# Kernel optimization log

Measured on AMD Instinct MI355X. Metric: run time of the kernel, lower is better.

## Reference

```python
import jax, jax.numpy as jnp
import numpy as np


def _gaussian_splat_map(mask, sigma_x, sigma_y):
    """Equivalent to the torch scatter loop: for every pixel (p,q) with mask>0,
    add exp(-((i-p)^2/(2 sx^2) + (j-q)^2/(2 sy^2))) into map[b]. Because the
    Gaussian is separable, the sum over sources is exactly Gx @ M @ Gy with
    full HxH / WxW Gaussian distance kernels. Then normalize by per-batch max
    (max==0 -> 1)."""
    B, H, W = mask.shape
    ih = jnp.arange(H, dtype=jnp.float32)
    iw = jnp.arange(W, dtype=jnp.float32)
    dx = ih[:, None] - ih[None, :]                      # (H, H): i - p
    dy = iw[:, None] - iw[None, :]                      # (W, W): q - j (symmetric)
    Gx = jnp.exp(-(dx * dx) / (2.0 * sigma_x * sigma_x))
    Gy = jnp.exp(-(dy * dy) / (2.0 * sigma_y * sigma_y))
    m = (mask > 0).astype(jnp.float32)                  # (B, H, W) source indicator
    g = jnp.einsum('ip,bpq,qj->bij', Gx, m, Gy)         # summed Gaussians per batch
    mx = jnp.max(g, axis=(1, 2), keepdims=True)
    mx = jnp.where(mx == 0, jnp.float32(1.0), mx)
    return g / mx


def setup_inputs() -> dict:
    key = jax.random.key(0)
    B, C, H, W = 64, 4, 256, 256
    x = jax.random.normal(key, (B, C, H, W), dtype=jnp.float32)
    return {"x": x}


def reference(x):
    # x: (B, 4, H, W) -> output: (B, 5, H, W) with history=True, mul=True
    ch0 = x[:, 0, :, :]
    target = _gaussian_splat_map(x[:, 2, :, :], 1.0, 1.0)
    cost = _gaussian_splat_map(x[:, 1, :, :], 1.0, 1.0)
    hist = _gaussian_splat_map(x[:, 3, :, :], 0.5, 0.5)
    mul = target * cost
    return jnp.stack([ch0, target, cost, hist, mul], axis=1)
```

## Files before the change

### kernel.cpp

```cpp
#include <hip/hip_runtime.h>
#include <cmath>

#define HH 256
#define WW 256
#define BB 64
#define RR 4
#define OROWS 16
#define TROWS (OROWS + 2*RR)
#define TSTR 260

static __device__ __forceinline__ float bin(float v) { return (v > 0.0f) ? 1.0f : 0.0f; }

__global__ __launch_bounds__(256) void splat_kernel(const float* __restrict__ x,
                                                    float* __restrict__ out,
                                                    float* __restrict__ maxws) {
    __shared__ float tmp[TROWS * TSTR];
    __shared__ float wred[4];

    const int strip = blockIdx.x;
    const int z = blockIdx.y;
    const int b = z / 3;
    const int m = z - 3 * b;
    const int src_c = (m == 0) ? 2 : ((m == 1) ? 1 : 3);
    const float inv2s2 = (m == 2) ? 2.0f : 0.5f;

    float w[RR + 1];
#pragma unroll
    for (int d = 0; d <= RR; ++d) w[d] = expf(-(float)(d * d) * inv2s2);

    const int ti0 = strip * OROWS;
    const float* xc = x + (((size_t)b * 4 + src_c) << 16);
    const int tid = threadIdx.x;

#pragma unroll
    for (int t = 0; t < 3; ++t) {
        int idx = tid + t * 256;
        int r = idx >> 5;
        int g = idx & 31;
        int gi = ti0 + r - RR;
        float4 q0 = make_float4(0.f,0.f,0.f,0.f), q1 = q0, q2 = q0, q3 = q0;
        if (gi >= 0 && gi < HH) {
            const float4* row = (const float4*)(xc + ((size_t)gi << 8));
            int i0 = (g > 0) ? (2 * g - 1) : 0;
            int i3 = (g < 31) ? (2 * g + 2) : 63;
            q0 = row[i0];
            q1 = row[2 * g];
            q2 = row[2 * g + 1];
            q3 = row[i3];
            if (g == 0)  q0 = make_float4(0.f,0.f,0.f,0.f);
            if (g == 31) q3 = make_float4(0.f,0.f,0.f,0.f);
        }
        float a[16] = {bin(q0.x), bin(q0.y), bin(q0.z), bin(q0.w),
                       bin(q1.x), bin(q1.y), bin(q1.z), bin(q1.w),
                       bin(q2.x), bin(q2.y), bin(q2.z), bin(q2.w),
                       bin(q3.x), bin(q3.y), bin(q3.z), bin(q3.w)};
        float o[8];
#pragma unroll
        for (int j = 0; j < 8; ++j) {
            o[j] = w[4] * (a[j]     + a[j + 8])
                 + w[3] * (a[j + 1] + a[j + 7])
                 + w[2] * (a[j + 2] + a[j + 6])
                 + w[1] * (a[j + 3] + a[j + 5])
                 + w[0] *  a[j + 4];
        }
        float* trow = &tmp[r * TSTR + 8 * g];
        *(float4*)trow       = make_float4(o[0], o[1], o[2], o[3]);
        *(float4*)(trow + 4) = make_float4(o[4], o[5], o[6], o[7]);
    }
    __syncthreads();

    const int c = tid & 63;
    const int gr = tid >> 6;
    float4 acc[4];
#pragma unroll
    for (int rr = 0; rr < 4; ++rr) acc[rr] = make_float4(0.f,0.f,0.f,0.f);
#pragma unroll
    for (int k = 0; k < 12; ++k) {
        float4 v = *(const float4*)&tmp[(4 * gr + k) * TSTR + 4 * c];
#pragma unroll
        for (int rr = 0; rr < 4; ++rr) {
            int d = k - RR - rr;
            if (d >= -RR && d <= RR) {
                float wk = w[d < 0 ? -d : d];
                acc[rr].x += wk * v.x; acc[rr].y += wk * v.y;
                acc[rr].z += wk * v.z; acc[rr].w += wk * v.w;
            }
        }
    }

    float* oc = out + (((size_t)b * 5 + (m + 1)) << 16);
    float lmax = 0.0f;
#pragma unroll
    for (int rr = 0; rr < 4; ++rr) {
        int row = ti0 + 4 * gr + rr;
        *(float4*)&oc[((size_t)row << 8) + 4 * c] = acc[rr];
        lmax = fmaxf(lmax, fmaxf(fmaxf(acc[rr].x, acc[rr].y), fmaxf(acc[rr].z, acc[rr].w)));
    }

#pragma unroll
    for (int off = 32; off > 0; off >>= 1)
        lmax = fmaxf(lmax, __shfl_down(lmax, off, 64));
    if ((tid & 63) == 0) wred[tid >> 6] = lmax;
    __syncthreads();
    if (tid == 0)
        maxws[z * 16 + strip] = fmaxf(fmaxf(wred[0], wred[1]), fmaxf(wred[2], wred[3]));
}

__global__ __launch_bounds__(256) void finalize_kernel(const float* __restrict__ x,
                                                       float* __restrict__ out,
                                                       const float* __restrict__ maxws) {
    __shared__ float lds[48];
    const int b = blockIdx.x >> 3;
    const int slab = blockIdx.x & 7;
    const int tid = threadIdx.x;

    if (tid < 48) lds[tid] = maxws[b * 48 + tid];
    __syncthreads();

    float mt = 0.f, mc = 0.f, mh = 0.f;
#pragma unroll
    for (int s = 0; s < 16; ++s) {
        mt = fmaxf(mt, lds[s]);
        mc = fmaxf(mc, lds[16 + s]);
        mh = fmaxf(mh, lds[32 + s]);
    }
    if (mt == 0.f) mt = 1.f;
    if (mc == 0.f) mc = 1.f;
    if (mh == 0.f) mh = 1.f;
    const float rt = 1.f / mt, rc = 1.f / mc, rh = 1.f / mh;

    const int plane4 = HH * WW / 4;
    const float4* x0 = (const float4*)(x + ((size_t)b * 4 << 16));
    float4* o = (float4*)(out + ((size_t)b * 5 << 16));

#pragma unroll
    for (int i = 0; i < 8; ++i) {
        int q = slab * 2048 + i * 256 + tid;
        float4 c0 = x0[q];
        float4 t = o[plane4 + q];
        float4 c = o[2 * plane4 + q];
        float4 h = o[3 * plane4 + q];
        t.x *= rt; t.y *= rt; t.z *= rt; t.w *= rt;
        c.x *= rc; c.y *= rc; c.z *= rc; c.w *= rc;
        h.x *= rh; h.y *= rh; h.z *= rh; h.w *= rh;
        float4 mul = make_float4(t.x * c.x, t.y * c.y, t.z * c.z, t.w * c.w);
        o[q] = c0;
        o[plane4 + q] = t;
        o[2 * plane4 + q] = c;
        o[3 * plane4 + q] = h;
        o[4 * plane4 + q] = mul;
    }
}

extern "C" void kernel_launch(void* const* d_in, const int* in_sizes, int n_in,
                              void* d_out, int out_size, void* d_ws, size_t ws_size,
                              hipStream_t stream) {
    const float* x = (const float*)d_in[0];
    float* out = (float*)d_out;
    float* maxws = (float*)d_ws;

    dim3 g1(HH / OROWS, BB * 3);
    hipLaunchKernelGGL(splat_kernel, g1, dim3(256), 0, stream, x, out, maxws);

    hipLaunchKernelGGL(finalize_kernel, dim3(BB * 8), dim3(256), 0, stream, x, out, maxws);
}
```

Baseline: 154.9 us.

## Stage unnormalized splat maps in bf16 workspace and enlarge row strips

The splat kernel now writes the unnormalized maps as bf16 into a separate workspace instead of fp32 into the output, which halves the intermediate write and read-back traffic between the two kernels. The finalize kernel reads the bf16 maps, normalizes them and writes all fp32 output planes once. Strips grow from 16 to 32 rows, which lowers the halo overhead per block but halves the number of blocks. Rounding to bf16 adds error of up to about 0.4% relative, which may fail tight tolerances.

New measurement: 156.7 us. Within noise of the previous version (+1.2%).

```diff
diff --git a/kernel.cpp b/kernel.cpp
--- a/kernel.cpp
+++ b/kernel.cpp
@@ -1,18 +1,30 @@
 #include <hip/hip_runtime.h>
+#include <hip/hip_bf16.h>
 #include <cmath>
 
 #define HH 256
 #define WW 256
 #define BB 64
 #define RR 4
-#define OROWS 16
+#define OROWS 32
+#define NSTRIP (HH / OROWS)
 #define TROWS (OROWS + 2*RR)
 #define TSTR 260
+#define MAPS_BYTES ((size_t)3 * BB * HH * WW * 2)
 
 static __device__ __forceinline__ float bin(float v) { return (v > 0.0f) ? 1.0f : 0.0f; }
 
+static __device__ __forceinline__ unsigned pk_bf16(float a, float b) {
+    __hip_bfloat162 h = __float22bfloat162_rn(make_float2(a, b));
+    return *reinterpret_cast<unsigned*>(&h);
+}
+static __device__ __forceinline__ float2 up_bf16(unsigned u) {
+    __hip_bfloat162 h = *reinterpret_cast<__hip_bfloat162*>(&u);
+    return __bfloat1622float2(h);
+}
+
 __global__ __launch_bounds__(256) void splat_kernel(const float* __restrict__ x,
-                                                    float* __restrict__ out,
+                                                    unsigned short* __restrict__ maps,
                                                     float* __restrict__ maxws) {
     __shared__ float tmp[TROWS * TSTR];
     __shared__ float wred[4];
@@ -33,7 +45,7 @@
     const int tid = threadIdx.x;
 
 #pragma unroll
-    for (int t = 0; t < 3; ++t) {
+    for (int t = 0; t < 5; ++t) {
         int idx = tid + t * 256;
         int r = idx >> 5;
         int g = idx & 31;
@@ -70,15 +82,15 @@
     __syncthreads();
 
     const int c = tid & 63;
-    const int gr = tid >> 6;
-    float4 acc[4];
+    const int wv = tid >> 6;
+    float4 acc[8];
 #pragma unroll
-    for (int rr = 0; rr < 4; ++rr) acc[rr] = make_float4(0.f,0.f,0.f,0.f);
+    for (int rr = 0; rr < 8; ++rr) acc[rr] = make_float4(0.f,0.f,0.f,0.f);
 #pragma unroll
-    for (int k = 0; k < 12; ++k) {
-        float4 v = *(const float4*)&tmp[(4 * gr + k) * TSTR + 4 * c];
+    for (int k = 0; k < 16; ++k) {
+        float4 v = *(const float4*)&tmp[(8 * wv + k) * TSTR + 4 * c];
 #pragma unroll
-        for (int rr = 0; rr < 4; ++rr) {
+        for (int rr = 0; rr < 8; ++rr) {
             int d = k - RR - rr;
             if (d >= -RR && d <= RR) {
                 float wk = w[d < 0 ? -d : d];
@@ -88,12 +100,13 @@
         }
     }
 
-    float* oc = out + (((size_t)b * 5 + (m + 1)) << 16);
+    unsigned short* mp = maps + ((size_t)z << 16);
     float lmax = 0.0f;
 #pragma unroll
-    for (int rr = 0; rr < 4; ++rr) {
-        int row = ti0 + 4 * gr + rr;
-        *(float4*)&oc[((size_t)row << 8) + 4 * c] = acc[rr];
+    for (int rr = 0; rr < 8; ++rr) {
+        int row = ti0 + 8 * wv + rr;
+        uint2 pk = make_uint2(pk_bf16(acc[rr].x, acc[rr].y), pk_bf16(acc[rr].z, acc[rr].w));
+        *(uint2*)&mp[(row << 8) + 4 * c] = pk;
         lmax = fmaxf(lmax, fmaxf(fmaxf(acc[rr].x, acc[rr].y), fmaxf(acc[rr].z, acc[rr].w)));
     }
 
@@ -103,26 +116,27 @@
     if ((tid & 63) == 0) wred[tid >> 6] = lmax;
     __syncthreads();
     if (tid == 0)
-        maxws[z * 16 + strip] = fmaxf(fmaxf(wred[0], wred[1]), fmaxf(wred[2], wred[3]));
+        maxws[z * NSTRIP + strip] = fmaxf(fmaxf(wred[0], wred[1]), fmaxf(wred[2], wred[3]));
 }
 
 __global__ __launch_bounds__(256) void finalize_kernel(const float* __restrict__ x,
                                                        float* __restrict__ out,
+                                                       const unsigned short* __restrict__ maps,
                                                        const float* __restrict__ maxws) {
-    __shared__ float lds[48];
+    __shared__ float lds[3 * NSTRIP];
     const int b = blockIdx.x >> 3;
     const int slab = blockIdx.x & 7;
     const int tid = threadIdx.x;
 
-    if (tid < 48) lds[tid] = maxws[b * 48 + tid];
+    if (tid < 3 * NSTRIP) lds[tid] = maxws[b * 3 * NSTRIP + tid];
     __syncthreads();
 
     float mt = 0.f, mc = 0.f, mh = 0.f;
 #pragma unroll
-    for (int s = 0; s < 16; ++s) {
+    for (int s = 0; s < NSTRIP; ++s) {
         mt = fmaxf(mt, lds[s]);
-        mc = fmaxf(mc, lds[16 + s]);
-        mh = fmaxf(mh, lds[32 + s]);
+        mc = fmaxf(mc, lds[NSTRIP + s]);
+        mh = fmaxf(mh, lds[2 * NSTRIP + s]);
     }
     if (mt == 0.f) mt = 1.f;
     if (mc == 0.f) mc = 1.f;
@@ -130,25 +144,37 @@
     const float rt = 1.f / mt, rc = 1.f / mc, rh = 1.f / mh;
 
     const int plane4 = HH * WW / 4;
+    const uint4* tp = (const uint4*)(maps + (((size_t)b * 3 + 0) << 16));
+    const uint4* cp = (const uint4*)(maps + (((size_t)b * 3 + 1) << 16));
+    const uint4* hp = (const uint4*)(maps + (((size_t)b * 3 + 2) << 16));
     const float4* x0 = (const float4*)(x + ((size_t)b * 4 << 16));
     float4* o = (float4*)(out + ((size_t)b * 5 << 16));
 
 #pragma unroll
-    for (int i = 0; i < 8; ++i) {
-        int q = slab * 2048 + i * 256 + tid;
-        float4 c0 = x0[q];
-        float4 t = o[plane4 + q];
-        float4 c = o[2 * plane4 + q];
-        float4 h = o[3 * plane4 + q];
-        t.x *= rt; t.y *= rt; t.z *= rt; t.w *= rt;
-        c.x *= rc; c.y *= rc; c.z *= rc; c.w *= rc;
-        h.x *= rh; h.y *= rh; h.z *= rh; h.w *= rh;
-        float4 mul = make_float4(t.x * c.x, t.y * c.y, t.z * c.z, t.w * c.w);
-        o[q] = c0;
-        o[plane4 + q] = t;
-        o[2 * plane4 + q] = c;
-        o[3 * plane4 + q] = h;
-        o[4 * plane4 + q] = mul;
+    for (int i = 0; i < 4; ++i) {
+        int q8 = slab * 1024 + i * 256 + tid;
+        uint4 tu = tp[q8], cu = cp[q8], hu = hp[q8];
+
+        float2 t0 = up_bf16(tu.x), t1 = up_bf16(tu.y), t2 = up_bf16(tu.z), t3 = up_bf16(tu.w);
+        float2 c0 = up_bf16(cu.x), c1 = up_bf16(cu.y), c2 = up_bf16(cu.z), c3 = up_bf16(cu.w);
+        float2 h0 = up_bf16(hu.x), h1 = up_bf16(hu.y), h2 = up_bf16(hu.z), h3 = up_bf16(hu.w);
+
+        float4 ta = make_float4(t0.x * rt, t0.y * rt, t1.x * rt, t1.y * rt);
+        float4 tb = make_float4(t2.x * rt, t2.y * rt, t3.x * rt, t3.y * rt);
+        float4 ca = make_float4(c0.x * rc, c0.y * rc, c1.x * rc, c1.y * rc);
+        float4 cb = make_float4(c2.x * rc, c2.y * rc, c3.x * rc, c3.y * rc);
+        float4 ha = make_float4(h0.x * rh, h0.y * rh, h1.x * rh, h1.y * rh);
+        float4 hb = make_float4(h2.x * rh, h2.y * rh, h3.x * rh, h3.y * rh);
+        float4 ma = make_float4(ta.x * ca.x, ta.y * ca.y, ta.z * ca.z, ta.w * ca.w);
+        float4 mb = make_float4(tb.x * cb.x, tb.y * cb.y, tb.z * cb.z, tb.w * cb.w);
+
+        int q = 2 * q8;
+        o[q]     = x0[q];
+        o[q + 1] = x0[q + 1];
+        o[plane4 + q]     = ta;  o[plane4 + q + 1]     = tb;
+        o[2 * plane4 + q] = ca;  o[2 * plane4 + q + 1] = cb;
+        o[3 * plane4 + q] = ha;  o[3 * plane4 + q + 1] = hb;
+        o[4 * plane4 + q] = ma;  o[4 * plane4 + q + 1] = mb;
     }
 }
 
@@ -157,10 +183,13 @@
                               hipStream_t stream) {
     const float* x = (const float*)d_in[0];
     float* out = (float*)d_out;
-    float* maxws = (float*)d_ws;
+    char* wsb = (char*)d_ws;
+    unsigned short* maps = (unsigned short*)wsb;
+    float* maxws = (float*)(wsb + MAPS_BYTES);
 
-    dim3 g1(HH / OROWS, BB * 3);
-    hipLaunchKernelGGL(splat_kernel, g1, dim3(256), 0, stream, x, out, maxws);
+    dim3 g1(NSTRIP, BB * 3);
+    hipLaunchKernelGGL(splat_kernel, g1, dim3(256), 0, stream, x, maps, maxws);
 
-    hipLaunchKernelGGL(finalize_kernel, dim3(BB * 8), dim3(256), 0, stream, x, out, maxws);
+    hipLaunchKernelGGL(finalize_kernel, dim3(BB * 8), dim3(256), 0, stream,
+                       x, out, maps, maxws);
 }
```

## Fuse splat and normalize into one kernel with grid-wide barrier

Applied to the files above, without the earlier changes.

Merges the three Gaussian-splat maps and the max-normalization/multiply pass into one kernel per (batch, strip) block. Results stay in registers while a global atomic-counter barrier waits for all per-strip maxima, so the intermediate maps are no longer written to and reread from global memory. Stencil radii are also shortened (3 for sigma 1, 2 for sigma 0.5), cutting LDS traffic and FMAs. It relies on all 1024 blocks being co-resident, with a guarded spin-wait, and uses an extra init launch to reset the counter.

Result: slower. 255.9 us (+65.1%).

```diff
diff --git a/kernel.cpp b/kernel.cpp
--- a/kernel.cpp
+++ b/kernel.cpp
@@ -4,151 +4,180 @@
 #define HH 256
 #define WW 256
 #define BB 64
-#define RR 4
 #define OROWS 16
-#define TROWS (OROWS + 2*RR)
+#define NSTRIP 16
 #define TSTR 260
+#define NBLK (BB * NSTRIP)
 
 static __device__ __forceinline__ float bin(float v) { return (v > 0.0f) ? 1.0f : 0.0f; }
 
-__global__ __launch_bounds__(256) void splat_kernel(const float* __restrict__ x,
-                                                    float* __restrict__ out,
-                                                    float* __restrict__ maxws) {
-    __shared__ float tmp[TROWS * TSTR];
-    __shared__ float wred[4];
+__global__ void init_kernel(unsigned* __restrict__ cnt) {
+    if (threadIdx.x == 0)
+        __hip_atomic_store(cnt, 0u, __ATOMIC_RELAXED, __HIP_MEMORY_SCOPE_AGENT);
+}
 
-    const int strip = blockIdx.x;
-    const int z = blockIdx.y;
-    const int b = z / 3;
-    const int m = z - 3 * b;
-    const int src_c = (m == 0) ? 2 : ((m == 1) ? 1 : 3);
-    const float inv2s2 = (m == 2) ? 2.0f : 0.5f;
+template<int R>
+static __device__ __forceinline__ void process_map(const float* __restrict__ xc,
+                                                   float* __restrict__ tmp,
+                                                   int ti0, int tid, int wv, int c,
+                                                   float inv2s2,
+                                                   float4 acc[4], float& lmax) {
+    float w[R + 1];
+#pragma unroll
+    for (int d = 0; d <= R; ++d) w[d] = expf(-(float)(d * d) * inv2s2);
 
-    float w[RR + 1];
-#pragma unroll
-    for (int d = 0; d <= RR; ++d) w[d] = expf(-(float)(d * d) * inv2s2);
-
-    const int ti0 = strip * OROWS;
-    const float* xc = x + (((size_t)b * 4 + src_c) << 16);
-    const int tid = threadIdx.x;
+    constexpr int TR = OROWS + 2 * R;
 
 #pragma unroll
-    for (int t = 0; t < 3; ++t) {
+    for (int t = 0; t < (TR * 32 + 255) / 256; ++t) {
         int idx = tid + t * 256;
-        int r = idx >> 5;
-        int g = idx & 31;
-        int gi = ti0 + r - RR;
-        float4 q0 = make_float4(0.f,0.f,0.f,0.f), q1 = q0, q2 = q0, q3 = q0;
-        if (gi >= 0 && gi < HH) {
-            const float4* row = (const float4*)(xc + ((size_t)gi << 8));
-            int i0 = (g > 0) ? (2 * g - 1) : 0;
-            int i3 = (g < 31) ? (2 * g + 2) : 63;
-            q0 = row[i0];
-            q1 = row[2 * g];
-            q2 = row[2 * g + 1];
-            q3 = row[i3];
-            if (g == 0)  q0 = make_float4(0.f,0.f,0.f,0.f);
-            if (g == 31) q3 = make_float4(0.f,0.f,0.f,0.f);
+        if (idx < TR * 32) {
+            int r = idx >> 5;
+            int g = idx & 31;
+            int gi = ti0 + r - R;
+            float4 q0 = make_float4(0.f,0.f,0.f,0.f), q1 = q0, q2 = q0, q3 = q0;
+            if (gi >= 0 && gi < HH) {
+                const float4* row = (const float4*)(xc + ((size_t)gi << 8));
+                int i0 = (g > 0) ? (2 * g - 1) : 0;
+                int i3 = (g < 31) ? (2 * g + 2) : 63;
+                q0 = row[i0];
+                q1 = row[2 * g];
+                q2 = row[2 * g + 1];
+                q3 = row[i3];
+                if (g == 0)  q0 = make_float4(0.f,0.f,0.f,0.f);
+                if (g == 31) q3 = make_float4(0.f,0.f,0.f,0.f);
+            }
+            float a[16] = {bin(q0.x), bin(q0.y), bin(q0.z), bin(q0.w),
+                           bin(q1.x), bin(q1.y), bin(q1.z), bin(q1.w),
+                           bin(q2.x), bin(q2.y), bin(q2.z), bin(q2.w),
+                           bin(q3.x), bin(q3.y), bin(q3.z), bin(q3.w)};
+            float o[8];
+#pragma unroll
+            for (int j = 0; j < 8; ++j) {
+                float s = w[0] * a[j + 4];
+#pragma unroll
+                for (int d = 1; d <= R; ++d)
+                    s += w[d] * (a[j + 4 - d] + a[j + 4 + d]);
+                o[j] = s;
+            }
+            float* trow = &tmp[r * TSTR + 8 * g];
+            *(float4*)trow       = make_float4(o[0], o[1], o[2], o[3]);
+            *(float4*)(trow + 4) = make_float4(o[4], o[5], o[6], o[7]);
         }
-        float a[16] = {bin(q0.x), bin(q0.y), bin(q0.z), bin(q0.w),
-                       bin(q1.x), bin(q1.y), bin(q1.z), bin(q1.w),
-                       bin(q2.x), bin(q2.y), bin(q2.z), bin(q2.w),
-                       bin(q3.x), bin(q3.y), bin(q3.z), bin(q3.w)};
-        float o[8];
-#pragma unroll
-        for (int j = 0; j < 8; ++j) {
-            o[j] = w[4] * (a[j]     + a[j + 8])
-                 + w[3] * (a[j + 1] + a[j + 7])
-                 + w[2] * (a[j + 2] + a[j + 6])
-                 + w[1] * (a[j + 3] + a[j + 5])
-                 + w[0] *  a[j + 4];
-        }
-        float* trow = &tmp[r * TSTR + 8 * g];
-        *(float4*)trow       = make_float4(o[0], o[1], o[2], o[3]);
-        *(float4*)(trow + 4) = make_float4(o[4], o[5], o[6], o[7]);
     }
     __syncthreads();
 
-    const int c = tid & 63;
-    const int gr = tid >> 6;
-    float4 acc[4];
 #pragma unroll
     for (int rr = 0; rr < 4; ++rr) acc[rr] = make_float4(0.f,0.f,0.f,0.f);
 #pragma unroll
-    for (int k = 0; k < 12; ++k) {
-        float4 v = *(const float4*)&tmp[(4 * gr + k) * TSTR + 4 * c];
+    for (int k = 0; k < 4 + 2 * R; ++k) {
+        float4 v = *(const float4*)&tmp[(4 * wv + k) * TSTR + 4 * c];
 #pragma unroll
         for (int rr = 0; rr < 4; ++rr) {
-            int d = k - RR - rr;
-            if (d >= -RR && d <= RR) {
+            int d = k - rr - R;
+            if (d >= -R && d <= R) {
                 float wk = w[d < 0 ? -d : d];
                 acc[rr].x += wk * v.x; acc[rr].y += wk * v.y;
                 acc[rr].z += wk * v.z; acc[rr].w += wk * v.w;
             }
         }
     }
+    lmax = 0.0f;
+#pragma unroll
+    for (int rr = 0; rr < 4; ++rr)
+        lmax = fmaxf(lmax, fmaxf(fmaxf(acc[rr].x, acc[rr].y),
+                                 fmaxf(acc[rr].z, acc[rr].w)));
+    __syncthreads();
+}
 
-    float* oc = out + (((size_t)b * 5 + (m + 1)) << 16);
-    float lmax = 0.0f;
+__global__ __launch_bounds__(256, 4) void fused_kernel(const float* __restrict__ x,
+                                                       float* __restrict__ out,
+                                                       float* __restrict__ maxws,
+                                                       unsigned* __restrict__ cnt) {
+    __shared__ float tmp[(OROWS + 6) * TSTR];
+    __shared__ float wred[12];
+
+    const int blk = blockIdx.x;
+    const int b = blk >> 4;
+    const int strip = blk & 15;
+    const int ti0 = strip * OROWS;
+    const int tid = threadIdx.x;
+    const int c = tid & 63;
+    const int wv = tid >> 6;
+
+    const float* xb = x + ((size_t)b * 4 << 16);
+    float4 acc[3][4];
+    float lmax[3];
+
+    process_map<3>(xb + (2 << 16), tmp, ti0, tid, wv, c, 0.5f, acc[0], lmax[0]);
+    process_map<3>(xb + (1 << 16), tmp, ti0, tid, wv, c, 0.5f, acc[1], lmax[1]);
+    process_map<2>(xb + (3 << 16), tmp, ti0, tid, wv, c, 2.0f, acc[2], lmax[2]);
+
+#pragma unroll
+    for (int m = 0; m < 3; ++m) {
+#pragma unroll
+        for (int off = 32; off > 0; off >>= 1)
+            lmax[m] = fmaxf(lmax[m], __shfl_down(lmax[m], off, 64));
+    }
+    if (c == 0) {
+        wred[wv * 3 + 0] = lmax[0];
+        wred[wv * 3 + 1] = lmax[1];
+        wred[wv * 3 + 2] = lmax[2];
+    }
+    __syncthreads();
+    if (tid < 3) {
+        float bm = fmaxf(fmaxf(wred[tid], wred[3 + tid]),
+                         fmaxf(wred[6 + tid], wred[9 + tid]));
+        __hip_atomic_store(&maxws[b * 48 + tid * 16 + strip], bm,
+                           __ATOMIC_RELAXED, __HIP_MEMORY_SCOPE_AGENT);
+    }
+
+    __syncthreads();
+    if (tid == 0) {
+        __threadfence();
+        __hip_atomic_fetch_add(cnt, 1u, __ATOMIC_RELEASE, __HIP_MEMORY_SCOPE_AGENT);
+        long guard = 0;
+        while (__hip_atomic_load(cnt, __ATOMIC_ACQUIRE, __HIP_MEMORY_SCOPE_AGENT) < NBLK
+               && ++guard < (1L << 24)) {  }
+    }
+    __syncthreads();
+
+    if (tid < 48)
+        tmp[tid] = __hip_atomic_load(&maxws[b * 48 + tid],
+                                     __ATOMIC_RELAXED, __HIP_MEMORY_SCOPE_AGENT);
+    __syncthreads();
+    float rmx[3];
+#pragma unroll
+    for (int m = 0; m < 3; ++m) {
+        float mx = 0.0f;
+#pragma unroll
+        for (int s = 0; s < 16; ++s) mx = fmaxf(mx, tmp[m * 16 + s]);
+        if (mx == 0.0f) mx = 1.0f;
+        rmx[m] = 1.0f / mx;
+    }
+
+    float* ob = out + ((size_t)b * 5 << 16);
 #pragma unroll
     for (int rr = 0; rr < 4; ++rr) {
-        int row = ti0 + 4 * gr + rr;
-        *(float4*)&oc[((size_t)row << 8) + 4 * c] = acc[rr];
-        lmax = fmaxf(lmax, fmaxf(fmaxf(acc[rr].x, acc[rr].y), fmaxf(acc[rr].z, acc[rr].w)));
+        int row = ti0 + 4 * wv + rr;
+        size_t off = ((size_t)row << 8) + 4 * c;
+        float4 t = acc[0][rr], cc = acc[1][rr], h = acc[2][rr];
+        t.x *= rmx[0]; t.y *= rmx[0]; t.z *= rmx[0]; t.w *= rmx[0];
+        cc.x *= rmx[1]; cc.y *= rmx[1]; cc.z *= rmx[1]; cc.w *= rmx[1];
+        h.x *= rmx[2]; h.y *= rmx[2]; h.z *= rmx[2]; h.w *= rmx[2];
+        float4 mul = make_float4(t.x * cc.x, t.y * cc.y, t.z * cc.z, t.w * cc.w);
+        *(float4*)&ob[(1 << 16) + off] = t;
+        *(float4*)&ob[(2 << 16) + off] = cc;
+        *(float4*)&ob[(3 << 16) + off] = h;
+        *(float4*)&ob[(4 << 16) + off] = mul;
     }
 
+    const float4* x0 = (const float4*)xb;
+    float4* o0 = (float4*)ob;
 #pragma unroll
-    for (int off = 32; off > 0; off >>= 1)
-        lmax = fmaxf(lmax, __shfl_down(lmax, off, 64));
-    if ((tid & 63) == 0) wred[tid >> 6] = lmax;
-    __syncthreads();
-    if (tid == 0)
-        maxws[z * 16 + strip] = fmaxf(fmaxf(wred[0], wred[1]), fmaxf(wred[2], wred[3]));
-}
-
-__global__ __launch_bounds__(256) void finalize_kernel(const float* __restrict__ x,
-                                                       float* __restrict__ out,
-                                                       const float* __restrict__ maxws) {
-    __shared__ float lds[48];
-    const int b = blockIdx.x >> 3;
-    const int slab = blockIdx.x & 7;
-    const int tid = threadIdx.x;
-
-    if (tid < 48) lds[tid] = maxws[b * 48 + tid];
-    __syncthreads();
-
-    float mt = 0.f, mc = 0.f, mh = 0.f;
-#pragma unroll
-    for (int s = 0; s < 16; ++s) {
-        mt = fmaxf(mt, lds[s]);
-        mc = fmaxf(mc, lds[16 + s]);
-        mh = fmaxf(mh, lds[32 + s]);
-    }
-    if (mt == 0.f) mt = 1.f;
-    if (mc == 0.f) mc = 1.f;
-    if (mh == 0.f) mh = 1.f;
-    const float rt = 1.f / mt, rc = 1.f / mc, rh = 1.f / mh;
-
-    const int plane4 = HH * WW / 4;
-    const float4* x0 = (const float4*)(x + ((size_t)b * 4 << 16));
-    float4* o = (float4*)(out + ((size_t)b * 5 << 16));
-
-#pragma unroll
-    for (int i = 0; i < 8; ++i) {
-        int q = slab * 2048 + i * 256 + tid;
-        float4 c0 = x0[q];
-        float4 t = o[plane4 + q];
-        float4 c = o[2 * plane4 + q];
-        float4 h = o[3 * plane4 + q];
-        t.x *= rt; t.y *= rt; t.z *= rt; t.w *= rt;
-        c.x *= rc; c.y *= rc; c.z *= rc; c.w *= rc;
-        h.x *= rh; h.y *= rh; h.z *= rh; h.w *= rh;
-        float4 mul = make_float4(t.x * c.x, t.y * c.y, t.z * c.z, t.w * c.w);
-        o[q] = c0;
-        o[plane4 + q] = t;
-        o[2 * plane4 + q] = c;
-        o[3 * plane4 + q] = h;
-        o[4 * plane4 + q] = mul;
+    for (int i = 0; i < 4; ++i) {
+        int q = strip * 1024 + i * 256 + tid;
+        o0[q] = x0[q];
     }
 }
 
@@ -158,9 +187,9 @@
     const float* x = (const float*)d_in[0];
     float* out = (float*)d_out;
     float* maxws = (float*)d_ws;
+    unsigned* cnt = (unsigned*)((char*)d_ws + 16384);
 
-    dim3 g1(HH / OROWS, BB * 3);
-    hipLaunchKernelGGL(splat_kernel, g1, dim3(256), 0, stream, x, out, maxws);
-
-    hipLaunchKernelGGL(finalize_kernel, dim3(BB * 8), dim3(256), 0, stream, x, out, maxws);
+    hipLaunchKernelGGL(init_kernel, dim3(1), dim3(64), 0, stream, cnt);
+    hipLaunchKernelGGL(fused_kernel, dim3(NBLK), dim3(256), 0, stream,
+                       x, out, maxws, cnt);
 }
```
